# Kernel optimization log

Hardware: AMD Instinct MI355X
Metric: run time of the kernel (lower is better)

## Reference

```python
import jax, jax.numpy as jnp
import numpy as np

N, E, G = 50000, 800000, 64   # nodes, edges, graphs
IN, HID, H = 128, 64, 4       # in_channels, hidden_channels, heads


def setup_inputs() -> dict:
    key = jax.random.key(0)
    ks = jax.random.split(key, 32)
    r = lambda i, shape, sc=0.05: jax.random.normal(ks[i], shape, jnp.float32) * sc
    inp = {
        "x": jax.random.normal(ks[0], (N, IN), jnp.float32),
        "edge_index": jax.random.randint(ks[1], (2, E), 0, N),
        "batch": jnp.sort(jax.random.randint(ks[2], (N,), 0, G)),
        # GATConv 1: in -> hidden, heads=4, concat
        "W1": r(3, (IN, H * HID)), "a_src1": r(4, (H, HID)), "a_dst1": r(5, (H, HID)), "b1": r(6, (H * HID,)),
        "bn1_g": 1.0 + r(7, (H * HID,)), "bn1_b": r(8, (H * HID,)), "bn1_m": r(9, (H * HID,)),
        "bn1_v": jax.random.uniform(ks[10], (H * HID,), jnp.float32, 0.5, 1.5),
        # GATConv 2: hidden*heads -> hidden, heads=4, concat
        "W2": r(11, (H * HID, H * HID)), "a_src2": r(12, (H, HID)), "a_dst2": r(13, (H, HID)), "b2": r(14, (H * HID,)),
        "bn2_g": 1.0 + r(15, (H * HID,)), "bn2_b": r(16, (H * HID,)), "bn2_m": r(17, (H * HID,)),
        "bn2_v": jax.random.uniform(ks[18], (H * HID,), jnp.float32, 0.5, 1.5),
        # GATConv 3: hidden*heads -> hidden, heads=1
        "W3": r(19, (H * HID, HID)), "a_src3": r(20, (1, HID)), "a_dst3": r(21, (1, HID)), "b3": r(22, (HID,)),
        # projection MLP: Linear(2*hidden, hidden) -> ReLU -> Linear(hidden, hidden)
        "P1": r(23, (2 * HID, HID)), "pb1": r(24, (HID,)),
        "P2": r(25, (HID, HID)), "pb2": r(26, (HID,)),
    }
    return inp


def _gat_conv(x, src, dst, n, W, a_s, a_d, b, concat):
    """PyG-style GATConv (eval mode). src/dst already include self-loops."""
    Hh, C = a_s.shape
    h = (x @ W).reshape(n, Hh, C)                       # [N, H, C]
    al_s = jnp.einsum('nhc,hc->nh', h, a_s)             # [N, H]
    al_d = jnp.einsum('nhc,hc->nh', h, a_d)             # [N, H]
    e = jax.nn.leaky_relu(al_s[src] + al_d[dst], 0.2)   # [E', H]
    # segment softmax over incoming edges of each dst node
    m = jax.ops.segment_max(e, dst, num_segments=n)     # [N, H] (finite: self-loops)
    ex = jnp.exp(e - m[dst])
    den = jax.ops.segment_sum(ex, dst, num_segments=n)
    alpha = ex / den[dst]                               # [E', H]
    out = jax.ops.segment_sum(h[src] * alpha[..., None], dst, num_segments=n)  # [N, H, C]
    out = out.reshape(n, Hh * C) if concat else out.mean(axis=1)
    return out + b


def _bn(x, g, b, m, v):
    return (x - m) * jax.lax.rsqrt(v + 1e-5) * g + b


def _forward(x, edge_index, batch,
             W1, a_src1, a_dst1, b1, bn1_g, bn1_b, bn1_m, bn1_v,
             W2, a_src2, a_dst2, b2, bn2_g, bn2_b, bn2_m, bn2_v,
             W3, a_src3, a_dst3, b3, P1, pb1, P2, pb2):
    n = x.shape[0]
    loop = jnp.arange(n)
    src = jnp.concatenate([edge_index[0], loop])        # add_self_loops=True
    dst = jnp.concatenate([edge_index[1], loop])
    h = _gat_conv(x, src, dst, n, W1, a_src1, a_dst1, b1, True)
    h = jax.nn.elu(_bn(h, bn1_g, bn1_b, bn1_m, bn1_v))  # dropout inactive in eval
    h = _gat_conv(h, src, dst, n, W2, a_src2, a_dst2, b2, True)
    h = jax.nn.elu(_bn(h, bn2_g, bn2_b, bn2_m, bn2_v))
    h = _gat_conv(h, src, dst, n, W3, a_src3, a_dst3, b3, False)  # heads=1
    x_max = jax.ops.segment_max(h, batch, num_segments=G)
    cnt = jax.ops.segment_sum(jnp.ones((n, 1), h.dtype), batch, num_segments=G)
    x_mean = jax.ops.segment_sum(h, batch, num_segments=G) / jnp.maximum(cnt, 1.0)
    z = jnp.concatenate([x_max, x_mean], axis=1)        # [G, 2*HID]
    z = jax.nn.relu(z @ P1 + pb1)
    return z @ P2 + pb2                                  # [G, HID]


def reference(x, edge_index, batch,
              W1, a_src1, a_dst1, b1, bn1_g, bn1_b, bn1_m, bn1_v,
              W2, a_src2, a_dst2, b2, bn2_g, bn2_b, bn2_m, bn2_v,
              W3, a_src3, a_dst3, b3, P1, pb1, P2, pb2):
    return _forward(x, edge_index, batch,
                    W1, a_src1, a_dst1, b1, bn1_g, bn1_b, bn1_m, bn1_v,
                    W2, a_src2, a_dst2, b2, bn2_g, bn2_b, bn2_m, bn2_v,
                    W3, a_src3, a_dst3, b3, P1, pb1, P2, pb2)
```

## Files before the change

### kernel.cpp

```cpp
#include <hip/hip_runtime.h>

typedef unsigned int uint;
typedef unsigned short ushort;

#define NFIX 50000
#define EFIX 800000
#define GFIX 64
#define BCAP 64
#define DCAP 128
#define WSTRIDE 136
#define PSL 16

__device__ __forceinline__ float bflo(uint u) { return __uint_as_float(u << 16); }
__device__ __forceinline__ float bfhi(uint u) { return __uint_as_float(u & 0xffff0000u); }
__device__ __forceinline__ float bf1(ushort u) { return __uint_as_float(((uint)u) << 16); }
__device__ __forceinline__ ushort f2bf(float f) {
    uint u = __float_as_uint(f);
    u += 0x7fffu + ((u >> 16) & 1u);
    return (ushort)(u >> 16);
}
__device__ __forceinline__ float lrelu(float x) { return fmaxf(x, 0.2f * x); }

typedef __attribute__((ext_vector_type(8))) short bf16x8;
typedef __attribute__((ext_vector_type(4))) float f32x4;
union U16B { uint4 u; bf16x8 v; };

__global__ void detect_idx_width(const int* __restrict__ ei, int* __restrict__ flag) {
    const int lane = threadIdx.x & 63;
    int v = (lane < 16) ? ei[2 * lane + 1] : 0;
    unsigned long long any = __ballot(v != 0);
    if (lane == 0 && blockIdx.x == 0) *flag = (any == 0ULL) ? 1 : 0;
}

__device__ __forceinline__ int ld_idx(const int* __restrict__ p, long i, int w64) {
    return w64 ? p[2 * i] : p[i];
}

__global__ void count_scatter(const int* __restrict__ ei, const int* __restrict__ flag,
                              int* __restrict__ cnt, int* __restrict__ ssb) {
    const int w64 = *flag;
    int e = blockIdx.x * 256 + threadIdx.x;
    if (e < EFIX) {
        int d = ld_idx(ei, (long)EFIX + e, w64);
        int s = ld_idx(ei, e, w64);
        int slot = atomicAdd(&cnt[d], 1);
        if (slot < BCAP) ssb[d * BCAP + slot] = s;
    }
}

#define XCNT 1600000
#define T1 (XCNT)
#define T2 (T1 + 128 * 256)
#define T3 (T2 + 256 * 256)
#define T4 (T3 + 256 * 64)
__global__ void prep(const float* __restrict__ x, ushort* __restrict__ xbf,
                     const float* __restrict__ W1, ushort* __restrict__ Wt1,
                     const float* __restrict__ W2, ushort* __restrict__ Wt2,
                     const float* __restrict__ W3, ushort* __restrict__ Wt3) {
    int i = blockIdx.x * 256 + threadIdx.x;
    if (i < XCNT) {
        int idx = i * 4;
        float4 v = *(const float4*)(x + idx);
        ushort4 o; o.x = f2bf(v.x); o.y = f2bf(v.y); o.z = f2bf(v.z); o.w = f2bf(v.w);
        *(ushort4*)(xbf + idx) = o;
    } else if (i < T2) {
        int j = i - T1; int k = j >> 8, c = j & 255;
        Wt1[c * 128 + k] = f2bf(W1[j]);
    } else if (i < T3) {
        int j = i - T2; int k = j >> 8, c = j & 255;
        Wt2[c * 256 + k] = f2bf(W2[j]);
    } else if (i < T4) {
        int j = i - T3; int k = j >> 6, c = j & 63;
        Wt3[c * 256 + k] = f2bf(W3[j]);
    }
}

template <int K>
__global__ __launch_bounds__(256) void gemm_mfma_nc256(const ushort* __restrict__ X,
                                                       const ushort* __restrict__ Wt,
                                                       const float* __restrict__ as_,
                                                       const float* __restrict__ ad_,
                                                       ushort* __restrict__ Hout,
                                                       float* __restrict__ als,
                                                       float* __restrict__ ald, int M) {
    const int wave = threadIdx.x >> 6;
    const int lane = threadIdx.x & 63;
    const int rowBase = blockIdx.x * 64;
    const int colBase = wave * 64;
    const int tr = lane & 15;
    const int kq = (lane >> 4) * 8;

    f32x4 acc[4][4];
#pragma unroll
    for (int i = 0; i < 4; ++i)
#pragma unroll
        for (int j = 0; j < 4; ++j) acc[i][j] = (f32x4){0.f, 0.f, 0.f, 0.f};

    const ushort* ap[4];
    const ushort* bp[4];
#pragma unroll
    for (int mi = 0; mi < 4; ++mi) {
        int r = rowBase + mi * 16 + tr;
        r = r < M ? r : M - 1;
        ap[mi] = X + (size_t)r * K + kq;
    }
#pragma unroll
    for (int ni = 0; ni < 4; ++ni)
        bp[ni] = Wt + (size_t)(colBase + ni * 16 + tr) * K + kq;

    for (int k0 = 0; k0 < K; k0 += 32) {
        bf16x8 a[4], b[4];
#pragma unroll
        for (int mi = 0; mi < 4; ++mi) { U16B t; t.u = *(const uint4*)(ap[mi] + k0); a[mi] = t.v; }
#pragma unroll
        for (int ni = 0; ni < 4; ++ni) { U16B t; t.u = *(const uint4*)(bp[ni] + k0); b[ni] = t.v; }
#pragma unroll
        for (int mi = 0; mi < 4; ++mi)
#pragma unroll
            for (int ni = 0; ni < 4; ++ni)
                acc[mi][ni] = __builtin_amdgcn_mfma_f32_16x16x32_bf16(a[mi], b[ni], acc[mi][ni], 0, 0, 0);
    }

    const int orow = (lane >> 4) * 4;
    const int ocol = colBase + tr;
#pragma unroll
    for (int mi = 0; mi < 4; ++mi) {
#pragma unroll
        for (int r = 0; r < 4; ++r) {
            int row = rowBase + mi * 16 + orow + r;
            if (row < M) {
#pragma unroll
                for (int ni = 0; ni < 4; ++ni)
                    Hout[(size_t)row * 256 + ocol + ni * 16] = f2bf(acc[mi][ni][r]);
            }
        }
    }

    float asv[4], adv[4];
#pragma unroll
    for (int ni = 0; ni < 4; ++ni) {
        asv[ni] = as_[wave * 64 + ni * 16 + tr];
        adv[ni] = ad_[wave * 64 + ni * 16 + tr];
    }
#pragma unroll
    for (int mi = 0; mi < 4; ++mi) {
#pragma unroll
        for (int r = 0; r < 4; ++r) {
            float ps = acc[mi][0][r] * asv[0] + acc[mi][1][r] * asv[1]
                     + acc[mi][2][r] * asv[2] + acc[mi][3][r] * asv[3];
            float pd = acc[mi][0][r] * adv[0] + acc[mi][1][r] * adv[1]
                     + acc[mi][2][r] * adv[2] + acc[mi][3][r] * adv[3];
#pragma unroll
            for (int off = 1; off < 16; off <<= 1) {
                ps += __shfl_xor(ps, off, 64);
                pd += __shfl_xor(pd, off, 64);
            }
            int row = rowBase + mi * 16 + orow + r;
            if (tr == 0 && row < M) {
                als[(size_t)row * 4 + wave] = ps;
                ald[(size_t)row * 4 + wave] = pd;
            }
        }
    }
}

template <int K, int NC, int HAL>
__global__ __launch_bounds__(256) void gemm_mfma(const ushort* __restrict__ X,
                                                 const ushort* __restrict__ Wt,
                                                 const float* __restrict__ as_,
                                                 const float* __restrict__ ad_,
                                                 ushort* __restrict__ Hout,
                                                 float* __restrict__ als,
                                                 float* __restrict__ ald, int M) {
    const int wave = threadIdx.x >> 6;
    const int lane = threadIdx.x & 63;
    const int rowBase = blockIdx.x * 256 + wave * 64;
    const int head = blockIdx.y;
    const int colBase = head * 64;
    const int tr = lane & 15;
    const int kq = (lane >> 4) * 8;

    f32x4 acc[4][4];
#pragma unroll
    for (int i = 0; i < 4; ++i)
#pragma unroll
        for (int j = 0; j < 4; ++j) acc[i][j] = (f32x4){0.f, 0.f, 0.f, 0.f};

    const ushort* ap[4];
    const ushort* bp[4];
#pragma unroll
    for (int mi = 0; mi < 4; ++mi) {
        int r = rowBase + mi * 16 + tr;
        r = r < M ? r : M - 1;
        ap[mi] = X + (size_t)r * K + kq;
    }
#pragma unroll
    for (int ni = 0; ni < 4; ++ni)
        bp[ni] = Wt + (size_t)(colBase + ni * 16 + tr) * K + kq;

    for (int k0 = 0; k0 < K; k0 += 32) {
        bf16x8 a[4], b[4];
#pragma unroll
        for (int mi = 0; mi < 4; ++mi) { U16B t; t.u = *(const uint4*)(ap[mi] + k0); a[mi] = t.v; }
#pragma unroll
        for (int ni = 0; ni < 4; ++ni) { U16B t; t.u = *(const uint4*)(bp[ni] + k0); b[ni] = t.v; }
#pragma unroll
        for (int mi = 0; mi < 4; ++mi)
#pragma unroll
            for (int ni = 0; ni < 4; ++ni)
                acc[mi][ni] = __builtin_amdgcn_mfma_f32_16x16x32_bf16(a[mi], b[ni], acc[mi][ni], 0, 0, 0);
    }

    const int orow = (lane >> 4) * 4;
    const int ocol = colBase + tr;
#pragma unroll
    for (int mi = 0; mi < 4; ++mi) {
#pragma unroll
        for (int r = 0; r < 4; ++r) {
            int row = rowBase + mi * 16 + orow + r;
            if (row < M) {
#pragma unroll
                for (int ni = 0; ni < 4; ++ni)
                    Hout[(size_t)row * NC + ocol + ni * 16] = f2bf(acc[mi][ni][r]);
            }
        }
    }

    float asv[4], adv[4];
#pragma unroll
    for (int ni = 0; ni < 4; ++ni) {
        asv[ni] = as_[head * 64 + ni * 16 + tr];
        adv[ni] = ad_[head * 64 + ni * 16 + tr];
    }
#pragma unroll
    for (int mi = 0; mi < 4; ++mi) {
#pragma unroll
        for (int r = 0; r < 4; ++r) {
            float ps = acc[mi][0][r] * asv[0] + acc[mi][1][r] * asv[1]
                     + acc[mi][2][r] * asv[2] + acc[mi][3][r] * asv[3];
            float pd = acc[mi][0][r] * adv[0] + acc[mi][1][r] * adv[1]
                     + acc[mi][2][r] * adv[2] + acc[mi][3][r] * adv[3];
#pragma unroll
            for (int off = 1; off < 16; off <<= 1) {
                ps += __shfl_xor(ps, off, 64);
                pd += __shfl_xor(pd, off, 64);
            }
            int row = rowBase + mi * 16 + orow + r;
            if (tr == 0 && row < M) {
                als[(size_t)row * HAL + head] = ps;
                ald[(size_t)row * HAL + head] = pd;
            }
        }
    }
}

template <int H_, int C, bool FINAL>
__global__ __launch_bounds__(256) void gat_gather(
    const ushort* __restrict__ hb, const float* __restrict__ als, const float* __restrict__ ald,
    const int* __restrict__ cnt, const int* __restrict__ ssb,
    const float* __restrict__ bias, const float* __restrict__ bng, const float* __restrict__ bnb,
    const float* __restrict__ bnm, const float* __restrict__ bnv,
    ushort* __restrict__ xnext, float* __restrict__ yout, int n) {
    constexpr int TC = H_ * C;
    constexpr int CPL = TC / 64;
    constexpr int GW = 64 / H_;
    constexpr int KMAX = DCAP / GW;
    constexpr int SHIFT = (TC == 256) ? 8 : 6;
    __shared__ float s_w[4][H_ * WSTRIDE];
    __shared__ int s_idx[4][DCAP];
    const int wv = threadIdx.x >> 6;
    const int node = blockIdx.x * 4 + wv;
    if (node >= n) return;
    const int lane = threadIdx.x & 63;
    const int head = lane / GW;
    const int hl = lane & (GW - 1);
    const int c0 = lane * CPL;

    const float aldn = ald[(size_t)node * H_ + head];
    const float selfle = lrelu(als[(size_t)node * H_ + head] + aldn);
    const int e0 = node * BCAP;
    int d = cnt[node];
    d = d < BCAP ? d : BCAP;

    float acc[CPL];

    {
        float le_reg[KMAX];
        int s_reg[KMAX];
        float m = selfle;
#pragma unroll
        for (int k = 0; k < KMAX; ++k) {
            int j = hl + k * GW;
            if (j < d) {
                int s = ssb[e0 + j];
                s_reg[k] = s;
                float le = lrelu(als[(size_t)s * H_ + head] + aldn);
                le_reg[k] = le;
                m = fmaxf(m, le);
            }
        }
#pragma unroll
        for (int off = 1; off < GW; off <<= 1) m = fmaxf(m, __shfl_xor(m, off, 64));

        float dsum = (hl == 0) ? __expf(selfle - m) : 0.f;
#pragma unroll
        for (int k = 0; k < KMAX; ++k) {
            int j = hl + k * GW;
            if (j < d) {
                float p = __expf(le_reg[k] - m);
                dsum += p;
                s_w[wv][head * WSTRIDE + j] = p;
                if (head == 0) s_idx[wv][j] = s_reg[k] << SHIFT;
            }
        }
#pragma unroll
        for (int off = 1; off < GW; off <<= 1) dsum += __shfl_xor(dsum, off, 64);
        const float inv = 1.0f / dsum;

        {
            float psf = __expf(selfle - m);
            if constexpr (CPL == 4) {
                uint2 hu = *(const uint2*)(hb + (size_t)node * TC + c0);
                acc[0] = psf * bflo(hu.x); acc[1] = psf * bfhi(hu.x);
                acc[2] = psf * bflo(hu.y); acc[3] = psf * bfhi(hu.y);
            } else {
                acc[0] = psf * bf1(hb[(size_t)node * TC + c0]);
            }
        }
        const float* wbase = &s_w[wv][head * WSTRIDE];
        const int* ibase = &s_idx[wv][0];
        const ushort* hc = hb + c0;
        int j = 0;
        for (; j + 8 <= d; j += 8) {
            float4 wa = *(const float4*)(wbase + j);
            float4 wb2 = *(const float4*)(wbase + j + 4);
            int4 ia = *(const int4*)(ibase + j);
            int4 ib = *(const int4*)(ibase + j + 4);
            if constexpr (CPL == 4) {
                uint2 h0 = *(const uint2*)(hc + ia.x);
                uint2 h1 = *(const uint2*)(hc + ia.y);
                uint2 h2 = *(const uint2*)(hc + ia.z);
                uint2 h3 = *(const uint2*)(hc + ia.w);
                uint2 h4 = *(const uint2*)(hc + ib.x);
                uint2 h5 = *(const uint2*)(hc + ib.y);
                uint2 h6 = *(const uint2*)(hc + ib.z);
                uint2 h7 = *(const uint2*)(hc + ib.w);
                acc[0] = fmaf(wa.x, bflo(h0.x), acc[0]); acc[1] = fmaf(wa.x, bfhi(h0.x), acc[1]);
                acc[2] = fmaf(wa.x, bflo(h0.y), acc[2]); acc[3] = fmaf(wa.x, bfhi(h0.y), acc[3]);
                acc[0] = fmaf(wa.y, bflo(h1.x), acc[0]); acc[1] = fmaf(wa.y, bfhi(h1.x), acc[1]);
                acc[2] = fmaf(wa.y, bflo(h1.y), acc[2]); acc[3] = fmaf(wa.y, bfhi(h1.y), acc[3]);
                acc[0] = fmaf(wa.z, bflo(h2.x), acc[0]); acc[1] = fmaf(wa.z, bfhi(h2.x), acc[1]);
                acc[2] = fmaf(wa.z, bflo(h2.y), acc[2]); acc[3] = fmaf(wa.z, bfhi(h2.y), acc[3]);
                acc[0] = fmaf(wa.w, bflo(h3.x), acc[0]); acc[1] = fmaf(wa.w, bfhi(h3.x), acc[1]);
                acc[2] = fmaf(wa.w, bflo(h3.y), acc[2]); acc[3] = fmaf(wa.w, bfhi(h3.y), acc[3]);
                acc[0] = fmaf(wb2.x, bflo(h4.x), acc[0]); acc[1] = fmaf(wb2.x, bfhi(h4.x), acc[1]);
                acc[2] = fmaf(wb2.x, bflo(h4.y), acc[2]); acc[3] = fmaf(wb2.x, bfhi(h4.y), acc[3]);
                acc[0] = fmaf(wb2.y, bflo(h5.x), acc[0]); acc[1] = fmaf(wb2.y, bfhi(h5.x), acc[1]);
                acc[2] = fmaf(wb2.y, bflo(h5.y), acc[2]); acc[3] = fmaf(wb2.y, bfhi(h5.y), acc[3]);
                acc[0] = fmaf(wb2.z, bflo(h6.x), acc[0]); acc[1] = fmaf(wb2.z, bfhi(h6.x), acc[1]);
                acc[2] = fmaf(wb2.z, bflo(h6.y), acc[2]); acc[3] = fmaf(wb2.z, bfhi(h6.y), acc[3]);
                acc[0] = fmaf(wb2.w, bflo(h7.x), acc[0]); acc[1] = fmaf(wb2.w, bfhi(h7.x), acc[1]);
                acc[2] = fmaf(wb2.w, bflo(h7.y), acc[2]); acc[3] = fmaf(wb2.w, bfhi(h7.y), acc[3]);
            } else {
                float h0 = bf1(hc[ia.x]), h1 = bf1(hc[ia.y]), h2 = bf1(hc[ia.z]), h3 = bf1(hc[ia.w]);
                float h4 = bf1(hc[ib.x]), h5 = bf1(hc[ib.y]), h6 = bf1(hc[ib.z]), h7 = bf1(hc[ib.w]);
                acc[0] = fmaf(wa.x, h0, acc[0]); acc[0] = fmaf(wa.y, h1, acc[0]);
                acc[0] = fmaf(wa.z, h2, acc[0]); acc[0] = fmaf(wa.w, h3, acc[0]);
                acc[0] = fmaf(wb2.x, h4, acc[0]); acc[0] = fmaf(wb2.y, h5, acc[0]);
                acc[0] = fmaf(wb2.z, h6, acc[0]); acc[0] = fmaf(wb2.w, h7, acc[0]);
            }
        }
        for (; j + 4 <= d; j += 4) {
            float4 wa = *(const float4*)(wbase + j);
            int4 ia = *(const int4*)(ibase + j);
            if constexpr (CPL == 4) {
                uint2 h0 = *(const uint2*)(hc + ia.x);
                uint2 h1 = *(const uint2*)(hc + ia.y);
                uint2 h2 = *(const uint2*)(hc + ia.z);
                uint2 h3 = *(const uint2*)(hc + ia.w);
                acc[0] = fmaf(wa.x, bflo(h0.x), acc[0]); acc[1] = fmaf(wa.x, bfhi(h0.x), acc[1]);
                acc[2] = fmaf(wa.x, bflo(h0.y), acc[2]); acc[3] = fmaf(wa.x, bfhi(h0.y), acc[3]);
                acc[0] = fmaf(wa.y, bflo(h1.x), acc[0]); acc[1] = fmaf(wa.y, bfhi(h1.x), acc[1]);
                acc[2] = fmaf(wa.y, bflo(h1.y), acc[2]); acc[3] = fmaf(wa.y, bfhi(h1.y), acc[3]);
                acc[0] = fmaf(wa.z, bflo(h2.x), acc[0]); acc[1] = fmaf(wa.z, bfhi(h2.x), acc[1]);
                acc[2] = fmaf(wa.z, bflo(h2.y), acc[2]); acc[3] = fmaf(wa.z, bfhi(h2.y), acc[3]);
                acc[0] = fmaf(wa.w, bflo(h3.x), acc[0]); acc[1] = fmaf(wa.w, bfhi(h3.x), acc[1]);
                acc[2] = fmaf(wa.w, bflo(h3.y), acc[2]); acc[3] = fmaf(wa.w, bfhi(h3.y), acc[3]);
            } else {
                float h0 = bf1(hc[ia.x]), h1 = bf1(hc[ia.y]), h2 = bf1(hc[ia.z]), h3 = bf1(hc[ia.w]);
                acc[0] = fmaf(wa.x, h0, acc[0]); acc[0] = fmaf(wa.y, h1, acc[0]);
                acc[0] = fmaf(wa.z, h2, acc[0]); acc[0] = fmaf(wa.w, h3, acc[0]);
            }
        }
        for (; j < d; ++j) {
            float w = wbase[j];
            int io = ibase[j];
            if constexpr (CPL == 4) {
                uint2 hu = *(const uint2*)(hc + io);
                acc[0] = fmaf(w, bflo(hu.x), acc[0]); acc[1] = fmaf(w, bfhi(hu.x), acc[1]);
                acc[2] = fmaf(w, bflo(hu.y), acc[2]); acc[3] = fmaf(w, bfhi(hu.y), acc[3]);
            } else {
                acc[0] = fmaf(w, bf1(hc[io]), acc[0]);
            }
        }
#pragma unroll
        for (int q = 0; q < CPL; ++q) acc[q] *= inv;
    }

    if constexpr (!FINAL) {
        float4 bi = *(const float4*)(bias + c0);
        float4 gg = *(const float4*)(bng + c0);
        float4 bb = *(const float4*)(bnb + c0);
        float4 mm = *(const float4*)(bnm + c0);
        float4 vv = *(const float4*)(bnv + c0);
        float biA[4] = { bi.x, bi.y, bi.z, bi.w };
        float ggA[4] = { gg.x, gg.y, gg.z, gg.w };
        float bbA[4] = { bb.x, bb.y, bb.z, bb.w };
        float mmA[4] = { mm.x, mm.y, mm.z, mm.w };
        float vvA[4] = { vv.x, vv.y, vv.z, vv.w };
        float r[4];
#pragma unroll
        for (int j2 = 0; j2 < 4; ++j2) {
            float v = acc[j2] + biA[j2];
            v = (v - mmA[j2]) * rsqrtf(vvA[j2] + 1e-5f) * ggA[j2] + bbA[j2];
            v = v > 0.f ? v : (__expf(v) - 1.0f);
            r[j2] = v;
        }
        uint p0 = (uint)f2bf(r[0]) | ((uint)f2bf(r[1]) << 16);
        uint p1 = (uint)f2bf(r[2]) | ((uint)f2bf(r[3]) << 16);
        uint2 o; o.x = p0; o.y = p1;
        *(uint2*)(xnext + (size_t)node * TC + c0) = o;
    } else {
        yout[(size_t)node * TC + c0] = acc[0] + bias[c0];
    }
}

__device__ __forceinline__ int lbound_w(const int* a, int n, int v, int w64) {
    int lo = 0, hi = n;
    while (lo < hi) {
        int mid = (lo + hi) >> 1;
        int bv = w64 ? a[2 * mid] : a[mid];
        if (bv < v) lo = mid + 1; else hi = mid;
    }
    return lo;
}

__global__ __launch_bounds__(256) void pool_part(const float* __restrict__ y, const int* __restrict__ batch,
                                                 const int* __restrict__ flag,
                                                 float* __restrict__ part) {
    const int w64 = *flag;
    const int g = blockIdx.x;
    const int sl = blockIdx.y;
    const int t = threadIdx.x;
    const int start = lbound_w(batch, NFIX, g, w64);
    const int end = lbound_w(batch, NFIX, g + 1, w64);
    const int len = end - start;
    const int s0 = start + (int)((long)len * sl / PSL);
    const int s1 = start + (int)((long)len * (sl + 1) / PSL);
    const int ch = t & 63, sub = t >> 6;
    float mx = -3.0e38f, sm = 0.f;
    for (int i = s0 + sub; i < s1; i += 4) {
        float v = y[(size_t)i * 64 + ch];
        mx = fmaxf(mx, v); sm += v;
    }
    __shared__ float smx[256], ssm[256];
    smx[t] = mx; ssm[t] = sm;
// ... 65 lines not shown
    const float* ad2 = (const float*)d_in[13];
    const float* b2 = (const float*)d_in[14];
    const float* bn2g = (const float*)d_in[15];
    const float* bn2b = (const float*)d_in[16];
    const float* bn2m = (const float*)d_in[17];
    const float* bn2v = (const float*)d_in[18];
    const float* W3 = (const float*)d_in[19];
    const float* as3 = (const float*)d_in[20];
    const float* ad3 = (const float*)d_in[21];
    const float* b3 = (const float*)d_in[22];
    const float* P1 = (const float*)d_in[23];
    const float* pb1 = (const float*)d_in[24];
    const float* P2 = (const float*)d_in[25];
    const float* pb2 = (const float*)d_in[26];
    float* out = (float*)d_out;
    (void)n_in; (void)out_size; (void)in_sizes;

    const int N_ = NFIX;
    const int E_ = EFIX;

    char* ws = (char*)d_ws;
    size_t off = 0;
    auto alloc = [&](size_t bytes) -> void* {
        void* p = ws + off;
        off = (off + bytes + 255) & ~(size_t)255;
        return p;
    };
    ushort* hbuf = (ushort*)alloc((size_t)N_ * 256 * 2);
    ushort* xbuf = (ushort*)alloc((size_t)N_ * 256 * 2);
    float* als = (float*)alloc((size_t)N_ * 4 * 4);
    float* ald = (float*)alloc((size_t)N_ * 4 * 4);
    int* cnt = (int*)alloc((size_t)N_ * 4);
    int* ssb = (int*)alloc((size_t)N_ * BCAP * 4);
    ushort* Wt1 = (ushort*)alloc(128 * 256 * 2);
    ushort* Wt2 = (ushort*)alloc(256 * 256 * 2);
    ushort* Wt3 = (ushort*)alloc(256 * 64 * 2);
    float* part = (float*)alloc((size_t)GFIX * PSL * 128 * 4);
    int* flag = (int*)alloc(256);
    ushort* xbf = xbuf;
    float* y3 = (float*)xbuf;
    const size_t needed = off;

    if (ws_size < needed) {
        write_code<<<1, 64, 0, stream>>>(out, 1000.0f + (float)(needed >> 20));
        return;
    }

    const int eg = (E_ + 255) / 256;
    const int ng4 = (N_ + 3) / 4;
    const int rb = (N_ + 255) / 256;
    const int rb64 = (N_ + 63) / 64;

    detect_idx_width<<<1, 64, 0, stream>>>(ei, flag);
    hipMemsetAsync(cnt, 0, (size_t)N_ * 4, stream);
    count_scatter<<<eg, 256, 0, stream>>>(ei, flag, cnt, ssb);

    prep<<<(T4 + 255) / 256, 256, 0, stream>>>(x, xbf, W1, Wt1, W2, Wt2, W3, Wt3);

    gemm_mfma_nc256<128><<<rb64, 256, 0, stream>>>(xbf, Wt1, as1, ad1, hbuf, als, ald, N_);
    gat_gather<4, 64, false><<<ng4, 256, 0, stream>>>(hbuf, als, ald, cnt, ssb,
                                                      b1, bn1g, bn1b, bn1m, bn1v, xbuf, nullptr, N_);
    gemm_mfma_nc256<256><<<rb64, 256, 0, stream>>>(xbuf, Wt2, as2, ad2, hbuf, als, ald, N_);
    gat_gather<4, 64, false><<<ng4, 256, 0, stream>>>(hbuf, als, ald, cnt, ssb,
                                                      b2, bn2g, bn2b, bn2m, bn2v, xbuf, nullptr, N_);
    gemm_mfma<256, 64, 1><<<dim3(rb, 1), 256, 0, stream>>>(xbuf, Wt3, as3, ad3, hbuf, als, ald, N_);
    gat_gather<1, 64, true><<<ng4, 256, 0, stream>>>(hbuf, als, ald, cnt, ssb,
                                                     b3, nullptr, nullptr, nullptr, nullptr,
                                                     nullptr, y3, N_);

    pool_part<<<dim3(GFIX, PSL), 256, 0, stream>>>(y3, batch, flag, part);
    pool_fin_mlp<<<GFIX, 64, 0, stream>>>(part, batch, flag, P1, pb1, P2, pb2, out);
}
```

Before: 426.1 us.

## Pack multiple nodes per wavefront in GAT gather with 16-byte feature loads

The GAT aggregation kernel now gives each lane 8 bf16 channels, loaded as one 16-byte access, instead of 4 or 1. One wavefront therefore covers 2 nodes in the 256-channel layers and 8 nodes in the 64-channel final layer, and grids shrink to match. This reduces idle lanes in the heads=1 layer and the number of load instructions per edge. In exchange, fewer lanes per head cooperate on the softmax, so each lane handles more edges serially. Out-of-range nodes are clamped to the last node and their results are not written, and launch bounds now request higher occupancy.

```diff
diff --git a/kernel.cpp b/kernel.cpp
--- a/kernel.cpp
+++ b/kernel.cpp
@@ -7,8 +7,7 @@
 #define EFIX 800000
 #define GFIX 64
 #define BCAP 64
-#define DCAP 128
-#define WSTRIDE 136
+#define WSTR 72
 #define PSL 16
 
 __device__ __forceinline__ float bflo(uint u) { return __uint_as_float(u << 16); }
@@ -254,184 +253,159 @@
     }
 }
 
-template <int H_, int C, bool FINAL>
-__global__ __launch_bounds__(256) void gat_gather(
+#define FMA8(W, H) \
+    acc[0] = fmaf(W, bflo(H.x), acc[0]); acc[1] = fmaf(W, bfhi(H.x), acc[1]); \
+    acc[2] = fmaf(W, bflo(H.y), acc[2]); acc[3] = fmaf(W, bfhi(H.y), acc[3]); \
+    acc[4] = fmaf(W, bflo(H.z), acc[4]); acc[5] = fmaf(W, bfhi(H.z), acc[5]); \
+    acc[6] = fmaf(W, bflo(H.w), acc[6]); acc[7] = fmaf(W, bfhi(H.w), acc[7])
+
+template <int H_, bool FINAL>
+__global__ __launch_bounds__(256, 8) void gat_gather(
     const ushort* __restrict__ hb, const float* __restrict__ als, const float* __restrict__ ald,
     const int* __restrict__ cnt, const int* __restrict__ ssb,
     const float* __restrict__ bias, const float* __restrict__ bng, const float* __restrict__ bnb,
     const float* __restrict__ bnm, const float* __restrict__ bnv,
     ushort* __restrict__ xnext, float* __restrict__ yout, int n) {
-    constexpr int TC = H_ * C;
-    constexpr int CPL = TC / 64;
-    constexpr int GW = 64 / H_;
-    constexpr int KMAX = DCAP / GW;
+    constexpr int TC = H_ * 64;
+    constexpr int CPL = 8;
+    constexpr int LPN = TC / CPL;
+    constexpr int NPW = 64 / LPN;
+    constexpr int NPB = 4 * NPW;
+    constexpr int GW = LPN / H_;
+    constexpr int KMAX = BCAP / GW;
     constexpr int SHIFT = (TC == 256) ? 8 : 6;
-    __shared__ float s_w[4][H_ * WSTRIDE];
-    __shared__ int s_idx[4][DCAP];
+    __shared__ __align__(16) float s_w[4][NPW][H_ * WSTR];
+    __shared__ __align__(16) int s_idx[4][NPW][WSTR];
     const int wv = threadIdx.x >> 6;
-    const int node = blockIdx.x * 4 + wv;
-    if (node >= n) return;
     const int lane = threadIdx.x & 63;
-    const int head = lane / GW;
-    const int hl = lane & (GW - 1);
-    const int c0 = lane * CPL;
-
-    const float aldn = ald[(size_t)node * H_ + head];
-    const float selfle = lrelu(als[(size_t)node * H_ + head] + aldn);
-    const int e0 = node * BCAP;
-    int d = cnt[node];
+    const int sub = lane / LPN;
+    const int ln = lane & (LPN - 1);
+    const int node = blockIdx.x * NPB + wv * NPW + sub;
+    const int nodec = node < n ? node : n - 1;
+    const int head = ln >> 3;
+    const int hl = ln & 7;
+    const int c0 = ln * CPL;
+
+    const float aldn = ald[(size_t)nodec * H_ + head];
+    const float selfle = lrelu(als[(size_t)nodec * H_ + head] + aldn);
+    const int e0 = nodec * BCAP;
+    int d = cnt[nodec];
     d = d < BCAP ? d : BCAP;
 
+    float le_reg[KMAX];
+    int s_reg[KMAX];
+    float m = selfle;
+#pragma unroll
+    for (int k = 0; k < KMAX; ++k) {
+        int j = hl + k * GW;
+        if (j < d) {
+            int s = ssb[e0 + j];
+            s_reg[k] = s;
+            float le = lrelu(als[(size_t)s * H_ + head] + aldn);
+            le_reg[k] = le;
+            m = fmaxf(m, le);
+        }
+    }
+#pragma unroll
+    for (int off = 1; off < GW; off <<= 1) m = fmaxf(m, __shfl_xor(m, off, 64));
+
+    float dsum = (hl == 0) ? __expf(selfle - m) : 0.f;
+#pragma unroll
+    for (int k = 0; k < KMAX; ++k) {
+        int j = hl + k * GW;
+        if (j < d) {
+            float p = __expf(le_reg[k] - m);
+            dsum += p;
+            s_w[wv][sub][head * WSTR + j] = p;
+            if (head == 0) s_idx[wv][sub][j] = s_reg[k] << SHIFT;
+        }
+    }
+#pragma unroll
+    for (int off = 1; off < GW; off <<= 1) dsum += __shfl_xor(dsum, off, 64);
+    const float inv = 1.0f / dsum;
+
     float acc[CPL];
-
     {
-        float le_reg[KMAX];
-        int s_reg[KMAX];
-        float m = selfle;
-#pragma unroll
-        for (int k = 0; k < KMAX; ++k) {
-            int j = hl + k * GW;
-            if (j < d) {
-                int s = ssb[e0 + j];
-                s_reg[k] = s;
-                float le = lrelu(als[(size_t)s * H_ + head] + aldn);
-                le_reg[k] = le;
-                m = fmaxf(m, le);
-            }
-        }
-#pragma unroll
-        for (int off = 1; off < GW; off <<= 1) m = fmaxf(m, __shfl_xor(m, off, 64));
-
-        float dsum = (hl == 0) ? __expf(selfle - m) : 0.f;
-#pragma unroll
-        for (int k = 0; k < KMAX; ++k) {
-            int j = hl + k * GW;
-            if (j < d) {
-                float p = __expf(le_reg[k] - m);
-                dsum += p;
-                s_w[wv][head * WSTRIDE + j] = p;
-                if (head == 0) s_idx[wv][j] = s_reg[k] << SHIFT;
-            }
-        }
-#pragma unroll
-        for (int off = 1; off < GW; off <<= 1) dsum += __shfl_xor(dsum, off, 64);
-        const float inv = 1.0f / dsum;
-
-        {
-            float psf = __expf(selfle - m);
-            if constexpr (CPL == 4) {
-                uint2 hu = *(const uint2*)(hb + (size_t)node * TC + c0);
-                acc[0] = psf * bflo(hu.x); acc[1] = psf * bfhi(hu.x);
-                acc[2] = psf * bflo(hu.y); acc[3] = psf * bfhi(hu.y);
-            } else {
-                acc[0] = psf * bf1(hb[(size_t)node * TC + c0]);
-            }
-        }
-        const float* wbase = &s_w[wv][head * WSTRIDE];
-        const int* ibase = &s_idx[wv][0];
-        const ushort* hc = hb + c0;
-        int j = 0;
-        for (; j + 8 <= d; j += 8) {
-            float4 wa = *(const float4*)(wbase + j);
-            float4 wb2 = *(const float4*)(wbase + j + 4);
-            int4 ia = *(const int4*)(ibase + j);
-            int4 ib = *(const int4*)(ibase + j + 4);
-            if constexpr (CPL == 4) {
-                uint2 h0 = *(const uint2*)(hc + ia.x);
-                uint2 h1 = *(const uint2*)(hc + ia.y);
-                uint2 h2 = *(const uint2*)(hc + ia.z);
-                uint2 h3 = *(const uint2*)(hc + ia.w);
-                uint2 h4 = *(const uint2*)(hc + ib.x);
-                uint2 h5 = *(const uint2*)(hc + ib.y);
-                uint2 h6 = *(const uint2*)(hc + ib.z);
-                uint2 h7 = *(const uint2*)(hc + ib.w);
-                acc[0] = fmaf(wa.x, bflo(h0.x), acc[0]); acc[1] = fmaf(wa.x, bfhi(h0.x), acc[1]);
-                acc[2] = fmaf(wa.x, bflo(h0.y), acc[2]); acc[3] = fmaf(wa.x, bfhi(h0.y), acc[3]);
-                acc[0] = fmaf(wa.y, bflo(h1.x), acc[0]); acc[1] = fmaf(wa.y, bfhi(h1.x), acc[1]);
-                acc[2] = fmaf(wa.y, bflo(h1.y), acc[2]); acc[3] = fmaf(wa.y, bfhi(h1.y), acc[3]);
-                acc[0] = fmaf(wa.z, bflo(h2.x), acc[0]); acc[1] = fmaf(wa.z, bfhi(h2.x), acc[1]);
-                acc[2] = fmaf(wa.z, bflo(h2.y), acc[2]); acc[3] = fmaf(wa.z, bfhi(h2.y), acc[3]);
-                acc[0] = fmaf(wa.w, bflo(h3.x), acc[0]); acc[1] = fmaf(wa.w, bfhi(h3.x), acc[1]);
-                acc[2] = fmaf(wa.w, bflo(h3.y), acc[2]); acc[3] = fmaf(wa.w, bfhi(h3.y), acc[3]);
-                acc[0] = fmaf(wb2.x, bflo(h4.x), acc[0]); acc[1] = fmaf(wb2.x, bfhi(h4.x), acc[1]);
-                acc[2] = fmaf(wb2.x, bflo(h4.y), acc[2]); acc[3] = fmaf(wb2.x, bfhi(h4.y), acc[3]);
-                acc[0] = fmaf(wb2.y, bflo(h5.x), acc[0]); acc[1] = fmaf(wb2.y, bfhi(h5.x), acc[1]);
-                acc[2] = fmaf(wb2.y, bflo(h5.y), acc[2]); acc[3] = fmaf(wb2.y, bfhi(h5.y), acc[3]);
-                acc[0] = fmaf(wb2.z, bflo(h6.x), acc[0]); acc[1] = fmaf(wb2.z, bfhi(h6.x), acc[1]);
-                acc[2] = fmaf(wb2.z, bflo(h6.y), acc[2]); acc[3] = fmaf(wb2.z, bfhi(h6.y), acc[3]);
-                acc[0] = fmaf(wb2.w, bflo(h7.x), acc[0]); acc[1] = fmaf(wb2.w, bfhi(h7.x), acc[1]);
-                acc[2] = fmaf(wb2.w, bflo(h7.y), acc[2]); acc[3] = fmaf(wb2.w, bfhi(h7.y), acc[3]);
-            } else {
-                float h0 = bf1(hc[ia.x]), h1 = bf1(hc[ia.y]), h2 = bf1(hc[ia.z]), h3 = bf1(hc[ia.w]);
-                float h4 = bf1(hc[ib.x]), h5 = bf1(hc[ib.y]), h6 = bf1(hc[ib.z]), h7 = bf1(hc[ib.w]);
-                acc[0] = fmaf(wa.x, h0, acc[0]); acc[0] = fmaf(wa.y, h1, acc[0]);
-                acc[0] = fmaf(wa.z, h2, acc[0]); acc[0] = fmaf(wa.w, h3, acc[0]);
-                acc[0] = fmaf(wb2.x, h4, acc[0]); acc[0] = fmaf(wb2.y, h5, acc[0]);
-                acc[0] = fmaf(wb2.z, h6, acc[0]); acc[0] = fmaf(wb2.w, h7, acc[0]);
-            }
-        }
-        for (; j + 4 <= d; j += 4) {
-            float4 wa = *(const float4*)(wbase + j);
-            int4 ia = *(const int4*)(ibase + j);
-            if constexpr (CPL == 4) {
-                uint2 h0 = *(const uint2*)(hc + ia.x);
-                uint2 h1 = *(const uint2*)(hc + ia.y);
-                uint2 h2 = *(const uint2*)(hc + ia.z);
-                uint2 h3 = *(const uint2*)(hc + ia.w);
-                acc[0] = fmaf(wa.x, bflo(h0.x), acc[0]); acc[1] = fmaf(wa.x, bfhi(h0.x), acc[1]);
-                acc[2] = fmaf(wa.x, bflo(h0.y), acc[2]); acc[3] = fmaf(wa.x, bfhi(h0.y), acc[3]);
-                acc[0] = fmaf(wa.y, bflo(h1.x), acc[0]); acc[1] = fmaf(wa.y, bfhi(h1.x), acc[1]);
-                acc[2] = fmaf(wa.y, bflo(h1.y), acc[2]); acc[3] = fmaf(wa.y, bfhi(h1.y), acc[3]);
-                acc[0] = fmaf(wa.z, bflo(h2.x), acc[0]); acc[1] = fmaf(wa.z, bfhi(h2.x), acc[1]);
-                acc[2] = fmaf(wa.z, bflo(h2.y), acc[2]); acc[3] = fmaf(wa.z, bfhi(h2.y), acc[3]);
-                acc[0] = fmaf(wa.w, bflo(h3.x), acc[0]); acc[1] = fmaf(wa.w, bfhi(h3.x), acc[1]);
-                acc[2] = fmaf(wa.w, bflo(h3.y), acc[2]); acc[3] = fmaf(wa.w, bfhi(h3.y), acc[3]);
-            } else {
-                float h0 = bf1(hc[ia.x]), h1 = bf1(hc[ia.y]), h2 = bf1(hc[ia.z]), h3 = bf1(hc[ia.w]);
-                acc[0] = fmaf(wa.x, h0, acc[0]); acc[0] = fmaf(wa.y, h1, acc[0]);
-                acc[0] = fmaf(wa.z, h2, acc[0]); acc[0] = fmaf(wa.w, h3, acc[0]);
-            }
-        }
-        for (; j < d; ++j) {
-            float w = wbase[j];
-            int io = ibase[j];
-            if constexpr (CPL == 4) {
-                uint2 hu = *(const uint2*)(hc + io);
-                acc[0] = fmaf(w, bflo(hu.x), acc[0]); acc[1] = fmaf(w, bfhi(hu.x), acc[1]);
-                acc[2] = fmaf(w, bflo(hu.y), acc[2]); acc[3] = fmaf(w, bfhi(hu.y), acc[3]);
-            } else {
-                acc[0] = fmaf(w, bf1(hc[io]), acc[0]);
-            }
-        }
-#pragma unroll
-        for (int q = 0; q < CPL; ++q) acc[q] *= inv;
-    }
+        float psf = __expf(selfle - m);
+        uint4 hs = *(const uint4*)(hb + (size_t)nodec * TC + c0);
+        acc[0] = psf * bflo(hs.x); acc[1] = psf * bfhi(hs.x);
+        acc[2] = psf * bflo(hs.y); acc[3] = psf * bfhi(hs.y);
+        acc[4] = psf * bflo(hs.z); acc[5] = psf * bfhi(hs.z);
+        acc[6] = psf * bflo(hs.w); acc[7] = psf * bfhi(hs.w);
+    }
+    const float* wbase = &s_w[wv][sub][head * WSTR];
+    const int* ibase = &s_idx[wv][sub][0];
+    const ushort* hc = hb + c0;
+    int j = 0;
+    for (; j + 8 <= d; j += 8) {
+        int4 ia = *(const int4*)(ibase + j);
+        int4 ib = *(const int4*)(ibase + j + 4);
+        uint4 h0 = *(const uint4*)(hc + ia.x);
+        uint4 h1 = *(const uint4*)(hc + ia.y);
+        uint4 h2 = *(const uint4*)(hc + ia.z);
+        uint4 h3 = *(const uint4*)(hc + ia.w);
+        uint4 h4 = *(const uint4*)(hc + ib.x);
+        uint4 h5 = *(const uint4*)(hc + ib.y);
+        uint4 h6 = *(const uint4*)(hc + ib.z);
+        uint4 h7 = *(const uint4*)(hc + ib.w);
+        float4 wa = *(const float4*)(wbase + j);
+        FMA8(wa.x, h0); FMA8(wa.y, h1); FMA8(wa.z, h2); FMA8(wa.w, h3);
+        float4 wb = *(const float4*)(wbase + j + 4);
+        FMA8(wb.x, h4); FMA8(wb.y, h5); FMA8(wb.z, h6); FMA8(wb.w, h7);
+    }
+    for (; j + 4 <= d; j += 4) {
+        int4 ia = *(const int4*)(ibase + j);
+        uint4 h0 = *(const uint4*)(hc + ia.x);
+        uint4 h1 = *(const uint4*)(hc + ia.y);
+        uint4 h2 = *(const uint4*)(hc + ia.z);
+        uint4 h3 = *(const uint4*)(hc + ia.w);
+        float4 wa = *(const float4*)(wbase + j);
+        FMA8(wa.x, h0); FMA8(wa.y, h1); FMA8(wa.z, h2); FMA8(wa.w, h3);
+    }
+    for (; j < d; ++j) {
+        float w = wbase[j];
+        uint4 h0 = *(const uint4*)(hc + ibase[j]);
+        FMA8(w, h0);
+    }
+#pragma unroll
+    for (int q = 0; q < CPL; ++q) acc[q] *= inv;
 
     if constexpr (!FINAL) {
-        float4 bi = *(const float4*)(bias + c0);
-        float4 gg = *(const float4*)(bng + c0);
-        float4 bb = *(const float4*)(bnb + c0);
-        float4 mm = *(const float4*)(bnm + c0);
-        float4 vv = *(const float4*)(bnv + c0);
-        float biA[4] = { bi.x, bi.y, bi.z, bi.w };
-        float ggA[4] = { gg.x, gg.y, gg.z, gg.w };
-        float bbA[4] = { bb.x, bb.y, bb.z, bb.w };
-        float mmA[4] = { mm.x, mm.y, mm.z, mm.w };
-        float vvA[4] = { vv.x, vv.y, vv.z, vv.w };
-        float r[4];
-#pragma unroll
-        for (int j2 = 0; j2 < 4; ++j2) {
-            float v = acc[j2] + biA[j2];
-            v = (v - mmA[j2]) * rsqrtf(vvA[j2] + 1e-5f) * ggA[j2] + bbA[j2];
+        float4 bi0 = *(const float4*)(bias + c0), bi1 = *(const float4*)(bias + c0 + 4);
+        float4 gg0 = *(const float4*)(bng + c0), gg1 = *(const float4*)(bng + c0 + 4);
+        float4 bb0 = *(const float4*)(bnb + c0), bb1 = *(const float4*)(bnb + c0 + 4);
+        float4 mm0 = *(const float4*)(bnm + c0), mm1 = *(const float4*)(bnm + c0 + 4);
+        float4 vv0 = *(const float4*)(bnv + c0), vv1 = *(const float4*)(bnv + c0 + 4);
+        float biA[8] = {bi0.x, bi0.y, bi0.z, bi0.w, bi1.x, bi1.y, bi1.z, bi1.w};
+        float ggA[8] = {gg0.x, gg0.y, gg0.z, gg0.w, gg1.x, gg1.y, gg1.z, gg1.w};
+        float bbA[8] = {bb0.x, bb0.y, bb0.z, bb0.w, bb1.x, bb1.y, bb1.z, bb1.w};
+        float mmA[8] = {mm0.x, mm0.y, mm0.z, mm0.w, mm1.x, mm1.y, mm1.z, mm1.w};
+        float vvA[8] = {vv0.x, vv0.y, vv0.z, vv0.w, vv1.x, vv1.y, vv1.z, vv1.w};
+        float r[8];
+#pragma unroll
+        for (int q = 0; q < 8; ++q) {
+            float v = acc[q] + biA[q];
+            v = (v - mmA[q]) * rsqrtf(vvA[q] + 1e-5f) * ggA[q] + bbA[q];
             v = v > 0.f ? v : (__expf(v) - 1.0f);
-            r[j2] = v;
-        }
-        uint p0 = (uint)f2bf(r[0]) | ((uint)f2bf(r[1]) << 16);
-        uint p1 = (uint)f2bf(r[2]) | ((uint)f2bf(r[3]) << 16);
-        uint2 o; o.x = p0; o.y = p1;
-        *(uint2*)(xnext + (size_t)node * TC + c0) = o;
+            r[q] = v;
+        }
+        if (node < n) {
+            uint4 o;
+            o.x = (uint)f2bf(r[0]) | ((uint)f2bf(r[1]) << 16);
+            o.y = (uint)f2bf(r[2]) | ((uint)f2bf(r[3]) << 16);
+            o.z = (uint)f2bf(r[4]) | ((uint)f2bf(r[5]) << 16);
+            o.w = (uint)f2bf(r[6]) | ((uint)f2bf(r[7]) << 16);
+            *(uint4*)(xnext + (size_t)node * TC + c0) = o;
+        }
     } else {
-        yout[(size_t)node * TC + c0] = acc[0] + bias[c0];
+        if (node < n) {
+            float4 o0 = {acc[0] + bias[c0 + 0], acc[1] + bias[c0 + 1],
+                         acc[2] + bias[c0 + 2], acc[3] + bias[c0 + 3]};
+            float4 o1 = {acc[4] + bias[c0 + 4], acc[5] + bias[c0 + 5],
+                         acc[6] + bias[c0 + 6], acc[7] + bias[c0 + 7]};
+            *(float4*)(yout + (size_t)node * TC + c0) = o0;
+            *(float4*)(yout + (size_t)node * TC + c0 + 4) = o1;
+        }
     }
 }
 
@@ -578,9 +552,10 @@
     }
 
     const int eg = (E_ + 255) / 256;
-    const int ng4 = (N_ + 3) / 4;
     const int rb = (N_ + 255) / 256;
     const int rb64 = (N_ + 63) / 64;
+    const int ng8 = (N_ + 7) / 8;
+    const int ng32 = (N_ + 31) / 32;
 
     detect_idx_width<<<1, 64, 0, stream>>>(ei, flag);
     hipMemsetAsync(cnt, 0, (size_t)N_ * 4, stream);
@@ -589,15 +564,15 @@
     prep<<<(T4 + 255) / 256, 256, 0, stream>>>(x, xbf, W1, Wt1, W2, Wt2, W3, Wt3);
 
     gemm_mfma_nc256<128><<<rb64, 256, 0, stream>>>(xbf, Wt1, as1, ad1, hbuf, als, ald, N_);
-    gat_gather<4, 64, false><<<ng4, 256, 0, stream>>>(hbuf, als, ald, cnt, ssb,
-                                                      b1, bn1g, bn1b, bn1m, bn1v, xbuf, nullptr, N_);
+    gat_gather<4, false><<<ng8, 256, 0, stream>>>(hbuf, als, ald, cnt, ssb,
+                                                  b1, bn1g, bn1b, bn1m, bn1v, xbuf, nullptr, N_);
     gemm_mfma_nc256<256><<<rb64, 256, 0, stream>>>(xbuf, Wt2, as2, ad2, hbuf, als, ald, N_);
-    gat_gather<4, 64, false><<<ng4, 256, 0, stream>>>(hbuf, als, ald, cnt, ssb,
-                                                      b2, bn2g, bn2b, bn2m, bn2v, xbuf, nullptr, N_);
+    gat_gather<4, false><<<ng8, 256, 0, stream>>>(hbuf, als, ald, cnt, ssb,
+                                                  b2, bn2g, bn2b, bn2m, bn2v, xbuf, nullptr, N_);
     gemm_mfma<256, 64, 1><<<dim3(rb, 1), 256, 0, stream>>>(xbuf, Wt3, as3, ad3, hbuf, als, ald, N_);
-    gat_gather<1, 64, true><<<ng4, 256, 0, stream>>>(hbuf, als, ald, cnt, ssb,
-                                                     b3, nullptr, nullptr, nullptr, nullptr,
-                                                     nullptr, y3, N_);
+    gat_gather<1, true><<<ng32, 256, 0, stream>>>(hbuf, als, ald, cnt, ssb,
+                                                  b3, nullptr, nullptr, nullptr, nullptr,
+                                                  nullptr, y3, N_);
 
     pool_part<<<dim3(GFIX, PSL), 256, 0, stream>>>(y3, batch, flag, part);
     pool_fin_mlp<<<GFIX, 64, 0, stream>>>(part, batch, flag, P1, pb1, P2, pb2, out);
```

Result: slower. 589.9 us (+38.4%).

## Stage activation tile in LDS and prepack weights in MFMA fragment order

Applied to the files above, without the earlier changes.

Weights are now pre-permuted during prep into MFMA fragment order, so each lane's B operand comes from one contiguous coalesced 16-byte load. The 64-row activation tile is copied into shared memory once per block and shared by all four waves, instead of each wave issuing strided global loads. The third-layer GEMM now uses 64-row blocks with each wave owning 16 columns, and it reduces the attention logits across waves through shared memory. The cost is more LDS per block (up to ~33KB), which may lower occupancy, plus a block-wide barrier before compute. The tile load reads past row M on the last block, which is safe only because the workspace buffer is larger than N rows.

```diff
diff --git a/kernel.cpp b/kernel.cpp
--- a/kernel.cpp
+++ b/kernel.cpp
@@ -53,10 +53,13 @@
 #define T2 (T1 + 128 * 256)
 #define T3 (T2 + 256 * 256)
 #define T4 (T3 + 256 * 64)
+__device__ __forceinline__ int frag_off(int k, int c, int K) {
+    return ((c >> 4) * (K >> 5) + (k >> 5)) * 512 + ((c & 15) + 16 * ((k >> 3) & 3)) * 8 + (k & 7);
+}
 __global__ void prep(const float* __restrict__ x, ushort* __restrict__ xbf,
-                     const float* __restrict__ W1, ushort* __restrict__ Wt1,
-                     const float* __restrict__ W2, ushort* __restrict__ Wt2,
-                     const float* __restrict__ W3, ushort* __restrict__ Wt3) {
+                     const float* __restrict__ W1, ushort* __restrict__ Wf1,
+                     const float* __restrict__ W2, ushort* __restrict__ Wf2,
+                     const float* __restrict__ W3, ushort* __restrict__ Wf3) {
     int i = blockIdx.x * 256 + threadIdx.x;
     if (i < XCNT) {
         int idx = i * 4;
@@ -65,149 +68,69 @@
         *(ushort4*)(xbf + idx) = o;
     } else if (i < T2) {
         int j = i - T1; int k = j >> 8, c = j & 255;
-        Wt1[c * 128 + k] = f2bf(W1[j]);
+        Wf1[frag_off(k, c, 128)] = f2bf(W1[j]);
     } else if (i < T3) {
         int j = i - T2; int k = j >> 8, c = j & 255;
-        Wt2[c * 256 + k] = f2bf(W2[j]);
+        Wf2[frag_off(k, c, 256)] = f2bf(W2[j]);
     } else if (i < T4) {
         int j = i - T3; int k = j >> 6, c = j & 63;
-        Wt3[c * 256 + k] = f2bf(W3[j]);
-    }
-}
-
-template <int K>
-__global__ __launch_bounds__(256) void gemm_mfma_nc256(const ushort* __restrict__ X,
-                                                       const ushort* __restrict__ Wt,
-                                                       const float* __restrict__ as_,
-                                                       const float* __restrict__ ad_,
-                                                       ushort* __restrict__ Hout,
-                                                       float* __restrict__ als,
-                                                       float* __restrict__ ald, int M) {
-    const int wave = threadIdx.x >> 6;
-    const int lane = threadIdx.x & 63;
-    const int rowBase = blockIdx.x * 64;
-    const int colBase = wave * 64;
-    const int tr = lane & 15;
-    const int kq = (lane >> 4) * 8;
-
-    f32x4 acc[4][4];
-#pragma unroll
-    for (int i = 0; i < 4; ++i)
-#pragma unroll
-        for (int j = 0; j < 4; ++j) acc[i][j] = (f32x4){0.f, 0.f, 0.f, 0.f};
-
-    const ushort* ap[4];
-    const ushort* bp[4];
-#pragma unroll
-    for (int mi = 0; mi < 4; ++mi) {
-        int r = rowBase + mi * 16 + tr;
-        r = r < M ? r : M - 1;
-        ap[mi] = X + (size_t)r * K + kq;
-    }
-#pragma unroll
-    for (int ni = 0; ni < 4; ++ni)
-        bp[ni] = Wt + (size_t)(colBase + ni * 16 + tr) * K + kq;
-
-    for (int k0 = 0; k0 < K; k0 += 32) {
-        bf16x8 a[4], b[4];
-#pragma unroll
-        for (int mi = 0; mi < 4; ++mi) { U16B t; t.u = *(const uint4*)(ap[mi] + k0); a[mi] = t.v; }
-#pragma unroll
-        for (int ni = 0; ni < 4; ++ni) { U16B t; t.u = *(const uint4*)(bp[ni] + k0); b[ni] = t.v; }
-#pragma unroll
-        for (int mi = 0; mi < 4; ++mi)
-#pragma unroll
-            for (int ni = 0; ni < 4; ++ni)
-                acc[mi][ni] = __builtin_amdgcn_mfma_f32_16x16x32_bf16(a[mi], b[ni], acc[mi][ni], 0, 0, 0);
-    }
-
-    const int orow = (lane >> 4) * 4;
-    const int ocol = colBase + tr;
-#pragma unroll
-    for (int mi = 0; mi < 4; ++mi) {
-#pragma unroll
-        for (int r = 0; r < 4; ++r) {
-            int row = rowBase + mi * 16 + orow + r;
-            if (row < M) {
-#pragma unroll
-                for (int ni = 0; ni < 4; ++ni)
-                    Hout[(size_t)row * 256 + ocol + ni * 16] = f2bf(acc[mi][ni][r]);
-            }
-        }
-    }
-
-    float asv[4], adv[4];
-#pragma unroll
-    for (int ni = 0; ni < 4; ++ni) {
-        asv[ni] = as_[wave * 64 + ni * 16 + tr];
-        adv[ni] = ad_[wave * 64 + ni * 16 + tr];
-    }
-#pragma unroll
-    for (int mi = 0; mi < 4; ++mi) {
-#pragma unroll
-        for (int r = 0; r < 4; ++r) {
-            float ps = acc[mi][0][r] * asv[0] + acc[mi][1][r] * asv[1]
-                     + acc[mi][2][r] * asv[2] + acc[mi][3][r] * asv[3];
-            float pd = acc[mi][0][r] * adv[0] + acc[mi][1][r] * adv[1]
-                     + acc[mi][2][r] * adv[2] + acc[mi][3][r] * adv[3];
-#pragma unroll
-            for (int off = 1; off < 16; off <<= 1) {
-                ps += __shfl_xor(ps, off, 64);
-                pd += __shfl_xor(pd, off, 64);
-            }
-            int row = rowBase + mi * 16 + orow + r;
-            if (tr == 0 && row < M) {
-                als[(size_t)row * 4 + wave] = ps;
-                ald[(size_t)row * 4 + wave] = pd;
-            }
-        }
-    }
-}
-
-template <int K, int NC, int HAL>
-__global__ __launch_bounds__(256) void gemm_mfma(const ushort* __restrict__ X,
-                                                 const ushort* __restrict__ Wt,
+        Wf3[frag_off(k, c, 256)] = f2bf(W3[j]);
+    }
+}
+
+template <int K, int NI, int HAL>
+__global__ __launch_bounds__(256) void gemm_frag(const ushort* __restrict__ X,
+                                                 const ushort* __restrict__ Wf,
                                                  const float* __restrict__ as_,
                                                  const float* __restrict__ ad_,
                                                  ushort* __restrict__ Hout,
                                                  float* __restrict__ als,
                                                  float* __restrict__ ald, int M) {
-    const int wave = threadIdx.x >> 6;
-    const int lane = threadIdx.x & 63;
-    const int rowBase = blockIdx.x * 256 + wave * 64;
-    const int head = blockIdx.y;
-    const int colBase = head * 64;
+    constexpr int NC = NI * 16 * 4;
+    constexpr int LOG2K = (K == 256) ? 8 : 7;
+    __shared__ ushort sa[64][K + 8];
+    __shared__ float s_ps[4][64];
+    __shared__ float s_pd[4][64];
+
+    const int tid = threadIdx.x;
+    const int wave = tid >> 6;
+    const int lane = tid & 63;
+    const int rowBase = blockIdx.x * 64;
+    const int colBase = wave * (NI * 16);
     const int tr = lane & 15;
     const int kq = (lane >> 4) * 8;
 
-    f32x4 acc[4][4];
+    const ushort* src = X + (size_t)rowBase * K;
+#pragma unroll
+    for (int it = 0; it < (64 * K) / 2048; ++it) {
+        int linear = it * 2048 + tid * 8;
+        int row = linear >> LOG2K;
+        int col = linear & (K - 1);
+        *(uint4*)(&sa[row][col]) = *(const uint4*)(src + linear);
+    }
+    __syncthreads();
+
+    f32x4 acc[4][NI];
 #pragma unroll
     for (int i = 0; i < 4; ++i)
 #pragma unroll
-        for (int j = 0; j < 4; ++j) acc[i][j] = (f32x4){0.f, 0.f, 0.f, 0.f};
-
-    const ushort* ap[4];
-    const ushort* bp[4];
-#pragma unroll
-    for (int mi = 0; mi < 4; ++mi) {
-        int r = rowBase + mi * 16 + tr;
-        r = r < M ? r : M - 1;
-        ap[mi] = X + (size_t)r * K + kq;
-    }
-#pragma unroll
-    for (int ni = 0; ni < 4; ++ni)
-        bp[ni] = Wt + (size_t)(colBase + ni * 16 + tr) * K + kq;
+        for (int j = 0; j < NI; ++j) acc[i][j] = (f32x4){0.f, 0.f, 0.f, 0.f};
+
+    const ushort* bp[NI];
+#pragma unroll
+    for (int ni = 0; ni < NI; ++ni)
+        bp[ni] = Wf + ((size_t)(colBase / 16 + ni) * (K / 32)) * 512 + lane * 8;
 
     for (int k0 = 0; k0 < K; k0 += 32) {
-        bf16x8 a[4], b[4];
-#pragma unroll
-        for (int mi = 0; mi < 4; ++mi) { U16B t; t.u = *(const uint4*)(ap[mi] + k0); a[mi] = t.v; }
-#pragma unroll
-        for (int ni = 0; ni < 4; ++ni) { U16B t; t.u = *(const uint4*)(bp[ni] + k0); b[ni] = t.v; }
+        bf16x8 a[4], b[NI];
+#pragma unroll
+        for (int mi = 0; mi < 4; ++mi) { U16B t; t.u = *(const uint4*)(&sa[mi * 16 + tr][k0 + kq]); a[mi] = t.v; }
+#pragma unroll
+        for (int ni = 0; ni < NI; ++ni) { U16B t; t.u = *(const uint4*)(bp[ni] + (k0 >> 5) * 512); b[ni] = t.v; }
 #pragma unroll
         for (int mi = 0; mi < 4; ++mi)
 #pragma unroll
-            for (int ni = 0; ni < 4; ++ni)
+            for (int ni = 0; ni < NI; ++ni)
                 acc[mi][ni] = __builtin_amdgcn_mfma_f32_16x16x32_bf16(a[mi], b[ni], acc[mi][ni], 0, 0, 0);
     }
 
@@ -220,35 +143,54 @@
             int row = rowBase + mi * 16 + orow + r;
             if (row < M) {
 #pragma unroll
-                for (int ni = 0; ni < 4; ++ni)
+                for (int ni = 0; ni < NI; ++ni)
                     Hout[(size_t)row * NC + ocol + ni * 16] = f2bf(acc[mi][ni][r]);
             }
         }
     }
 
-    float asv[4], adv[4];
-#pragma unroll
-    for (int ni = 0; ni < 4; ++ni) {
-        asv[ni] = as_[head * 64 + ni * 16 + tr];
-        adv[ni] = ad_[head * 64 + ni * 16 + tr];
+    float asv[NI], adv[NI];
+#pragma unroll
+    for (int ni = 0; ni < NI; ++ni) {
+        asv[ni] = as_[colBase + ni * 16 + tr];
+        adv[ni] = ad_[colBase + ni * 16 + tr];
     }
 #pragma unroll
     for (int mi = 0; mi < 4; ++mi) {
 #pragma unroll
         for (int r = 0; r < 4; ++r) {
-            float ps = acc[mi][0][r] * asv[0] + acc[mi][1][r] * asv[1]
-                     + acc[mi][2][r] * asv[2] + acc[mi][3][r] * asv[3];
-            float pd = acc[mi][0][r] * adv[0] + acc[mi][1][r] * adv[1]
-                     + acc[mi][2][r] * adv[2] + acc[mi][3][r] * adv[3];
+            float ps = 0.f, pd = 0.f;
+#pragma unroll
+            for (int ni = 0; ni < NI; ++ni) {
+                ps += acc[mi][ni][r] * asv[ni];
+                pd += acc[mi][ni][r] * adv[ni];
+            }
 #pragma unroll
             for (int off = 1; off < 16; off <<= 1) {
                 ps += __shfl_xor(ps, off, 64);
                 pd += __shfl_xor(pd, off, 64);
             }
-            int row = rowBase + mi * 16 + orow + r;
-            if (tr == 0 && row < M) {
-                als[(size_t)row * HAL + head] = ps;
-                ald[(size_t)row * HAL + head] = pd;
+            if constexpr (HAL == 4) {
+                int row = rowBase + mi * 16 + orow + r;
+                if (tr == 0 && row < M) {
+                    als[(size_t)row * 4 + wave] = ps;
+                    ald[(size_t)row * 4 + wave] = pd;
+                }
+            } else {
+                if (tr == 0) {
+                    s_ps[wave][mi * 16 + orow + r] = ps;
+                    s_pd[wave][mi * 16 + orow + r] = pd;
+                }
+            }
+        }
+    }
+    if constexpr (HAL == 1) {
+        __syncthreads();
+        if (tid < 64) {
+            int row = rowBase + tid;
+            if (row < M) {
+                als[row] = s_ps[0][tid] + s_ps[1][tid] + s_ps[2][tid] + s_ps[3][tid];
+                ald[row] = s_pd[0][tid] + s_pd[1][tid] + s_pd[2][tid] + s_pd[3][tid];
             }
         }
     }
@@ -563,9 +505,9 @@
     float* ald = (float*)alloc((size_t)N_ * 4 * 4);
     int* cnt = (int*)alloc((size_t)N_ * 4);
     int* ssb = (int*)alloc((size_t)N_ * BCAP * 4);
-    ushort* Wt1 = (ushort*)alloc(128 * 256 * 2);
-    ushort* Wt2 = (ushort*)alloc(256 * 256 * 2);
-    ushort* Wt3 = (ushort*)alloc(256 * 64 * 2);
+    ushort* Wf1 = (ushort*)alloc(128 * 256 * 2);
+    ushort* Wf2 = (ushort*)alloc(256 * 256 * 2);
+    ushort* Wf3 = (ushort*)alloc(256 * 64 * 2);
     float* part = (float*)alloc((size_t)GFIX * PSL * 128 * 4);
     int* flag = (int*)alloc(256);
     ushort* xbf = xbuf;
@@ -579,22 +521,21 @@
 
     const int eg = (E_ + 255) / 256;
     const int ng4 = (N_ + 3) / 4;
-    const int rb = (N_ + 255) / 256;
     const int rb64 = (N_ + 63) / 64;
 
     detect_idx_width<<<1, 64, 0, stream>>>(ei, flag);
     hipMemsetAsync(cnt, 0, (size_t)N_ * 4, stream);
     count_scatter<<<eg, 256, 0, stream>>>(ei, flag, cnt, ssb);
 
-    prep<<<(T4 + 255) / 256, 256, 0, stream>>>(x, xbf, W1, Wt1, W2, Wt2, W3, Wt3);
-
-    gemm_mfma_nc256<128><<<rb64, 256, 0, stream>>>(xbf, Wt1, as1, ad1, hbuf, als, ald, N_);
+    prep<<<(T4 + 255) / 256, 256, 0, stream>>>(x, xbf, W1, Wf1, W2, Wf2, W3, Wf3);
+
+    gemm_frag<128, 4, 4><<<rb64, 256, 0, stream>>>(xbf, Wf1, as1, ad1, hbuf, als, ald, N_);
     gat_gather<4, 64, false><<<ng4, 256, 0, stream>>>(hbuf, als, ald, cnt, ssb,
                                                       b1, bn1g, bn1b, bn1m, bn1v, xbuf, nullptr, N_);
-    gemm_mfma_nc256<256><<<rb64, 256, 0, stream>>>(xbuf, Wt2, as2, ad2, hbuf, als, ald, N_);
+    gemm_frag<256, 4, 4><<<rb64, 256, 0, stream>>>(xbuf, Wf2, as2, ad2, hbuf, als, ald, N_);
     gat_gather<4, 64, false><<<ng4, 256, 0, stream>>>(hbuf, als, ald, cnt, ssb,
                                                       b2, bn2g, bn2b, bn2m, bn2v, xbuf, nullptr, N_);
-    gemm_mfma<256, 64, 1><<<dim3(rb, 1), 256, 0, stream>>>(xbuf, Wt3, as3, ad3, hbuf, als, ald, N_);
+    gemm_frag<256, 1, 1><<<rb64, 256, 0, stream>>>(xbuf, Wf3, as3, ad3, hbuf, als, ald, N_);
     gat_gather<1, 64, true><<<ng4, 256, 0, stream>>>(hbuf, als, ald, cnt, ssb,
                                                      b3, nullptr, nullptr, nullptr, nullptr,
                                                      nullptr, y3, N_);
```

Result: faster. 407.2 us (-4.4%).
